# Kernel tuning notes

Measured on AMD Instinct MI355X. Metric: run time of the kernel, lower is better.

## Reference

```python
import jax, jax.numpy as jnp
import numpy as np

B, H, S, D = 2, 12, 2048, 64


def setup_inputs() -> dict:
    key = jax.random.key(0)
    kq, kk, kv = jax.random.split(key, 3)
    q = jax.random.normal(kq, (B, H, S, D), dtype=jnp.float32)
    k = jax.random.normal(kk, (B, H, S, D), dtype=jnp.float32)
    v = jax.random.normal(kv, (B, H, S, D), dtype=jnp.float32)
    # causal mask: True = attend (keep), lower triangle
    mask = jnp.tril(jnp.ones((S, S), dtype=bool))
    return {"q": q, "k": k, "v": v, "mask": mask}


def reference(q, k, v, mask):
    dim = q.shape[-1]
    # [B,H,S,S] scores
    scores = jnp.einsum("bhqd,bhkd->bhqk", q, k) / jnp.sqrt(jnp.asarray(dim, q.dtype))
    # dynamic mask-direction logic from the original module:
    # if the mask is denser in the strict upper triangle, True means "mask out";
    # otherwise True means "keep".
    sq = mask.shape[-1]
    sample = mask.reshape(-1, sq, sq)[0]
    upper = jnp.triu(jnp.ones_like(sample, dtype=bool), k=1)
    flip = jnp.sum(sample & upper) > jnp.sum(sample & ~upper)
    keep = jnp.where(flip, ~mask, mask)  # True = keep
    neg_inf = jnp.asarray(-jnp.inf, scores.dtype)
    scores = jnp.where(keep, scores, neg_inf)
    weights = jax.nn.softmax(scores, axis=-1)
    # dropout with p_drop=0.0 is the identity
    return jnp.einsum("bhqk,bhkd->bhqd", weights, v)
```

## Files before the change

kernel.cpp:

```cpp
#include <hip/hip_runtime.h>
#include <hip/hip_bf16.h>


#define SEQ 2048
#define DH 64
#define NHEADS 24
#define BN 64
#define LDK 72
#define ELEMS_PER_TENSOR (NHEADS * SEQ * DH)
#define NSLOT5 (NHEADS * 16 * 4)
#define WS_BF16  ((size_t)3 * ELEMS_PER_TENSOR * 2)
#define WS_FA5   (WS_BF16 + (size_t)NSLOT5 * 8192 * 4 + (size_t)NSLOT5 * 128 * 4)

typedef float f32x4 __attribute__((ext_vector_type(4)));
typedef __bf16 bf16x8 __attribute__((ext_vector_type(8)));
typedef __bf16 bf16x4 __attribute__((ext_vector_type(4)));

#if __has_builtin(__builtin_amdgcn_exp2f)
#define EXP2F(x) __builtin_amdgcn_exp2f(x)
#else
#define EXP2F(x) exp2f(x)
#endif

#define QSCALE 0.1803368801111204f

__global__ __launch_bounds__(256)
void prep_kernel(const float* __restrict__ q, const float* __restrict__ k,
                 const float* __restrict__ v,
                 __bf16* __restrict__ qs, __bf16* __restrict__ ks,
                 __bf16* __restrict__ vt)
{
    __shared__ __bf16 T[64][LDK];
    const int bx = blockIdx.x;
    const int tid = threadIdx.x;
    if (bx < 3072) {
        const int t = bx * 256 + tid;
        const int half = ELEMS_PER_TENSOR / 8;
        const bool is_q = t < half;
        const int idx = (is_q ? t : t - half) * 8;
        const float* src = is_q ? q : k;
        const float sc = is_q ? QSCALE : 1.0f;
        f32x4 a = *(const f32x4*)(src + idx);
        f32x4 b = *(const f32x4*)(src + idx + 4);
        bf16x8 o;
        #pragma unroll
        for (int j = 0; j < 4; ++j) { o[j] = (__bf16)(a[j] * sc); o[4 + j] = (__bf16)(b[j] * sc); }
        *(bf16x8*)((is_q ? qs : ks) + idx) = o;
    } else {
        const int b2 = bx - 3072;
        const int bh = b2 >> 5;
        const int s0 = (b2 & 31) * 64;
        const int r = tid >> 2, c0 = (tid & 3) * 16;
        const float* vp = v + (size_t)bh * SEQ * DH + (size_t)(s0 + r) * DH + c0;
        __bf16 tmp[16];
        #pragma unroll
        for (int jj = 0; jj < 16; ++jj) tmp[jj] = (__bf16)vp[jj];
        *(bf16x8*)&T[r][c0]     = *(bf16x8*)&tmp[0];
        *(bf16x8*)&T[r][c0 + 8] = *(bf16x8*)&tmp[8];
        __syncthreads();
        const int d = tid >> 2, j0 = (tid & 3) * 16;
        __bf16 o[16];
        #pragma unroll
        for (int jj = 0; jj < 16; ++jj) o[jj] = T[j0 + jj][d];
        __bf16* op = vt + (size_t)bh * DH * SEQ + (size_t)d * SEQ + s0 + j0;
        *(bf16x8*)op       = *(bf16x8*)&o[0];
        *(bf16x8*)(op + 8) = *(bf16x8*)&o[8];
    }
}

__global__ __launch_bounds__(256, 4)
void fa5_kernel(const __bf16* __restrict__ qs, const __bf16* __restrict__ ks,
                const __bf16* __restrict__ vt,
                float* __restrict__ opart, float* __restrict__ lpart)
{
    const int bx = blockIdx.x;
    const int bh = bx / 40;
    const int rem = 39 - (bx % 40);
    int mt2, st;
    if      (rem >= 36) { mt2 = 15; st = 36; }
    else if (rem >= 32) { mt2 = 14; st = 32; }
    else if (rem >= 28) { mt2 = 13; st = 28; }
    else if (rem >= 24) { mt2 = 12; st = 24; }
    else if (rem >= 21) { mt2 = 11; st = 21; }
    else if (rem >= 18) { mt2 = 10; st = 18; }
    else if (rem >= 15) { mt2 = 9;  st = 15; }
    else if (rem >= 12) { mt2 = 8;  st = 12; }
    else if (rem >= 10) { mt2 = 7;  st = 10; }
    else if (rem >= 8)  { mt2 = 6;  st = 8; }
    else if (rem >= 6)  { mt2 = 5;  st = 6; }
    else if (rem >= 4)  { mt2 = 4;  st = 4; }
    else                { mt2 = rem; st = rem; }
    const int chunk = rem - st;
    const int jt0 = chunk * 8;
    const int jt_end = min(jt0 + 8, 2 * mt2 + 2);
    const int q0 = mt2 * 128;

    const int tid = threadIdx.x;
    const int w = tid >> 6, lane = tid & 63;
    const int g = lane >> 4, li = lane & 15;

    __shared__ __bf16 Ks[64 * 64];
    __shared__ __bf16 Vs[64 * 64];
    __shared__ __bf16 Ps[4 * 32 * 64];

    const __bf16* qh = qs + (size_t)bh * SEQ * DH;
    const __bf16* kh = ks + (size_t)bh * SEQ * DH;
    const __bf16* vh = vt + (size_t)bh * DH * SEQ;

    bf16x8 qf[2][2];
    #pragma unroll
    for (int a = 0; a < 2; ++a) {
        const __bf16* qp = qh + (size_t)(q0 + w * 32 + a * 16 + li) * DH + g * 8;
        qf[a][0] = *(const bf16x8*)qp;
        qf[a][1] = *(const bf16x8*)(qp + 32);
    }

    bf16x8 ones;
    #pragma unroll
    for (int j = 0; j < 8; ++j) ones[j] = (__bf16)1.0f;

    f32x4 acc[2][4] = {};
    f32x4 accl[2] = {};

    const int srow0 = tid >> 3;
    const int sg    = tid & 7;

    bf16x8 kr[2], vr[2];
    #pragma unroll
    for (int s = 0; s < 2; ++s) {
        const int row = s * 32 + srow0;
        const int lg = sg ^ (row & 7);
        kr[s] = *(const bf16x8*)(kh + (size_t)(jt0 * BN + row) * DH + lg * 8);
        vr[s] = *(const bf16x8*)(vh + (size_t)row * SEQ + jt0 * BN + lg * 8);
    }
    #pragma unroll
    for (int s = 0; s < 2; ++s) {
        *(bf16x8*)((char*)Ks + s * 4096 + tid * 16) = kr[s];
        *(bf16x8*)((char*)Vs + s * 4096 + tid * 16) = vr[s];
    }
    __syncthreads();

    for (int jt = jt0; jt < jt_end; ++jt) {
        if (jt + 1 < jt_end) {
            const int kv1 = (jt + 1) * BN;
            #pragma unroll
            for (int s = 0; s < 2; ++s) {
                const int row = s * 32 + srow0;
                const int lg = sg ^ (row & 7);
                kr[s] = *(const bf16x8*)(kh + (size_t)(kv1 + row) * DH + lg * 8);
                vr[s] = *(const bf16x8*)(vh + (size_t)row * SEQ + kv1 + lg * 8);
            }
        }

        float s4[2][4][4];
        #pragma unroll
        for (int t = 0; t < 4; ++t) {
            f32x4 sa0 = {}, sa1 = {};
            #pragma unroll
            for (int c = 0; c < 2; ++c) {
                bf16x8 kf = *(const bf16x8*)((const char*)Ks +
                    (t * 16 + li) * 128 + (((c * 4 + g) ^ (li & 7)) << 4));
                sa0 = __builtin_amdgcn_mfma_f32_16x16x32_bf16(kf, qf[0][c], sa0, 0, 0, 0);
                sa1 = __builtin_amdgcn_mfma_f32_16x16x32_bf16(kf, qf[1][c], sa1, 0, 0, 0);
            }
            #pragma unroll
            for (int r = 0; r < 4; ++r) { s4[0][t][r] = sa0[r]; s4[1][t][r] = sa1[r]; }
        }

        if (jt >= 2 * mt2) {
            #pragma unroll
            for (int a = 0; a < 2; ++a) {
                const int qr = q0 + w * 32 + a * 16 + li;
                #pragma unroll
                for (int t = 0; t < 4; ++t) {
                    #pragma unroll
                    for (int r = 0; r < 4; ++r)
                        if (jt * 64 + t * 16 + g * 4 + r > qr) s4[a][t][r] = -1e30f;
                }
            }
        }

        #pragma unroll
        for (int a = 0; a < 2; ++a) {
            const int row = a * 16 + li;
            #pragma unroll
            for (int t = 0; t < 4; ++t) {
                bf16x4 p4;
                #pragma unroll
                for (int r = 0; r < 4; ++r) p4[r] = (__bf16)EXP2F(s4[a][t][r]);
                const int pg = (t * 2 + (g >> 1)) ^ (li & 7);
                *(bf16x4*)((char*)Ps + w * 4096 + row * 128 + (pg << 4) + ((g & 1) << 3)) = p4;
            }
        }

        #pragma unroll
        for (int c = 0; c < 2; ++c) {
            const int pgp = ((c * 4 + g) ^ (li & 7)) << 4;
            bf16x8 pf0 = *(const bf16x8*)((const char*)Ps + w * 4096 + li * 128 + pgp);
            bf16x8 pf1 = *(const bf16x8*)((const char*)Ps + w * 4096 + (16 + li) * 128 + pgp);
            accl[0] = __builtin_amdgcn_mfma_f32_16x16x32_bf16(pf0, ones, accl[0], 0, 0, 0);
            accl[1] = __builtin_amdgcn_mfma_f32_16x16x32_bf16(pf1, ones, accl[1], 0, 0, 0);
            #pragma unroll
            for (int t = 0; t < 4; ++t) {
                bf16x8 vf = *(const bf16x8*)((const char*)Vs +
                    (t * 16 + li) * 128 + pgp);
                acc[0][t] = __builtin_amdgcn_mfma_f32_16x16x32_bf16(pf0, vf, acc[0][t], 0, 0, 0);
                acc[1][t] = __builtin_amdgcn_mfma_f32_16x16x32_bf16(pf1, vf, acc[1][t], 0, 0, 0);
            }
        }

        if (jt + 1 < jt_end) {
            __syncthreads();
            #pragma unroll
            for (int s = 0; s < 2; ++s) {
                *(bf16x8*)((char*)Ks + s * 4096 + tid * 16) = kr[s];
                *(bf16x8*)((char*)Vs + s * 4096 + tid * 16) = vr[s];
            }
            __syncthreads();
        }
    }

    const int slot = (bh * 16 + mt2) * 4 + chunk;
    float* po = opart + (size_t)slot * 8192;
    #pragma unroll
    for (int a = 0; a < 2; ++a) {
        #pragma unroll
        for (int r = 0; r < 4; ++r) {
            const int row = w * 32 + a * 16 + g * 4 + r;
            float* op = po + row * 64 + li;
            #pragma unroll
            for (int t = 0; t < 4; ++t) op[t * 16] = acc[a][t][r];
            if (li == 0) lpart[(size_t)slot * 128 + row] = accl[a][r];
        }
    }
}

__global__ __launch_bounds__(256)
void fa_reduce(const float* __restrict__ opart, const float* __restrict__ lpart,
               float* __restrict__ out)
{
    const int bx = blockIdx.x;
    const int bh = bx >> 4, mt2 = bx & 15;
    const int nc = (mt2 >> 2) + 1;
    const int base = (bh * 16 + mt2) * 4;
    const int tid = threadIdx.x;
    #pragma unroll
    for (int rnd = 0; rnd < 8; ++rnd) {
        const int flat = rnd * 1024 + tid * 4;
        const int row = flat >> 6;
        f32x4 o = {};
        float l = 0.0f;
        for (int c = 0; c < nc; ++c) {
            o += *(const f32x4*)(opart + (size_t)(base + c) * 8192 + flat);
            l += lpart[(size_t)(base + c) * 128 + row];
        }
        const float inv = 1.0f / l;
        f32x4 res = { o[0] * inv, o[1] * inv, o[2] * inv, o[3] * inv };
        *(f32x4*)(out + (size_t)bh * SEQ * DH + (size_t)mt2 * 8192 + flat) = res;
    }
}

__global__ __launch_bounds__(256, 2)
void fa_causal_kernel(const float* __restrict__ q, const float* __restrict__ k,
                      const float* __restrict__ v, float* __restrict__ out)
{
    const int mt = 31 - (blockIdx.x & 31);
    const int bh = blockIdx.x >> 5;
    const int tid = threadIdx.x;
    const int w = tid >> 6, lane = tid & 63;
    const int g = lane >> 4, li = lane & 15;
    const int m0 = mt * 64;
    __shared__ __bf16 KsF[BN][LDK];
    __shared__ __bf16 VsF[DH][LDK];
    __shared__ __bf16 PsF[4][16][LDK];
    const size_t head_off = (size_t)bh * SEQ * DH;
    const float* qh = q + head_off;
    const float* kh = k + head_off;
    const float* vh = v + head_off;
    float* oh = out + head_off;
    const int qrow = m0 + w * 16 + li;
    bf16x8 qf[2];
    {
        const float* qp = qh + (size_t)qrow * DH + g * 8;
        #pragma unroll
        for (int c = 0; c < 2; ++c) {
            const float* p = qp + c * 32;
            #pragma unroll
            for (int jj = 0; jj < 8; ++jj) qf[c][jj] = (__bf16)p[jj];
        }
    }
    f32x4 acc[4] = {};
    float mrow[4], lrow[4];
    #pragma unroll
    for (int r = 0; r < 4; ++r) { mrow[r] = -1e30f; lrow[r] = 0.0f; }
    const float scale = 0.125f;
    const int srow = tid >> 2, scol = (tid & 3) * 16;
    for (int jt = 0; jt <= mt; ++jt) {
        const int kv0 = jt * BN;
        __syncthreads();
        {
            const float* kp = kh + (size_t)(kv0 + srow) * DH + scol;
            __bf16 tmp[16];
            #pragma unroll
            for (int jj = 0; jj < 16; ++jj) tmp[jj] = (__bf16)kp[jj];
            *(bf16x8*)&KsF[srow][scol]     = *(bf16x8*)&tmp[0];
            *(bf16x8*)&KsF[srow][scol + 8] = *(bf16x8*)&tmp[8];
            const float* vp = vh + (size_t)(kv0 + srow) * DH + scol;
            #pragma unroll
            for (int jj = 0; jj < 16; ++jj) VsF[scol + jj][srow] = (__bf16)vp[jj];
        }
        __syncthreads();
        float s4[4][4];
        #pragma unroll
        for (int t = 0; t < 4; ++t) {
            f32x4 sa = {};
            #pragma unroll
            for (int c = 0; c < 2; ++c) {
                bf16x8 kfr = *(const bf16x8*)&KsF[t * 16 + li][c * 32 + g * 8];
                sa = __builtin_amdgcn_mfma_f32_16x16x32_bf16(qf[c], kfr, sa, 0, 0, 0);
            }
            #pragma unroll
            for (int r = 0; r < 4; ++r) s4[t][r] = sa[r] * scale;
        }
        if (jt == mt) {
            #pragma unroll
            for (int t = 0; t < 4; ++t) {
                const int col = kv0 + t * 16 + li;
                #pragma unroll
                for (int r = 0; r < 4; ++r)
                    if (col > m0 + w * 16 + g * 4 + r) s4[t][r] = -1e30f;
            }
        }
        #pragma unroll
        for (int r = 0; r < 4; ++r) {
            float mx = fmaxf(fmaxf(s4[0][r], s4[1][r]), fmaxf(s4[2][r], s4[3][r]));
            #pragma unroll
            for (int off = 1; off < 16; off <<= 1)
                mx = fmaxf(mx, __shfl_xor(mx, off, 64));
            const float mnew = fmaxf(mrow[r], mx);
            const float alpha = __expf(mrow[r] - mnew);
            mrow[r] = mnew;
            float ps = 0.0f;
            #pragma unroll
            for (int t = 0; t < 4; ++t) {
                const float p = __expf(s4[t][r] - mnew);
                s4[t][r] = p;
                ps += p;
            }
            #pragma unroll
            for (int off = 1; off < 16; off <<= 1)
                ps += __shfl_xor(ps, off, 64);
            lrow[r] = lrow[r] * alpha + ps;
            #pragma unroll
            for (int t = 0; t < 4; ++t) acc[t][r] *= alpha;
        }
        #pragma unroll
        for (int t = 0; t < 4; ++t)
            #pragma unroll
            for (int r = 0; r < 4; ++r)
                PsF[w][g * 4 + r][t * 16 + li] = (__bf16)s4[t][r];
        __syncthreads();
        #pragma unroll
        for (int c = 0; c < 2; ++c) {
            bf16x8 pf = *(const bf16x8*)&PsF[w][li][c * 32 + g * 8];
            #pragma unroll
            for (int t = 0; t < 4; ++t) {
                bf16x8 vfr = *(const bf16x8*)&VsF[t * 16 + li][c * 32 + g * 8];
                acc[t] = __builtin_amdgcn_mfma_f32_16x16x32_bf16(pf, vfr, acc[t], 0, 0, 0);
            }
        }
    }
    #pragma unroll
    for (int r = 0; r < 4; ++r) {
        const int row = m0 + w * 16 + g * 4 + r;
        const float inv = 1.0f / lrow[r];
        float* op = oh + (size_t)row * DH + li;
        #pragma unroll
        for (int t = 0; t < 4; ++t) op[t * 16] = acc[t][r] * inv;
    }
}

extern "C" void kernel_launch(void* const* d_in, const int* in_sizes, int n_in,
                              void* d_out, int out_size, void* d_ws, size_t ws_size,
                              hipStream_t stream) {
    (void)in_sizes; (void)n_in; (void)out_size;
    const float* q = (const float*)d_in[0];
    const float* k = (const float*)d_in[1];
    const float* v = (const float*)d_in[2];
    float* out = (float*)d_out;

    if (ws_size >= WS_FA5) {
        __bf16* qs = (__bf16*)d_ws;
        __bf16* ks = qs + ELEMS_PER_TENSOR;
        __bf16* vt = ks + ELEMS_PER_TENSOR;
        float* opart = (float*)((char*)d_ws + WS_BF16);
        float* lpart = opart + (size_t)NSLOT5 * 8192;
        prep_kernel<<<dim3(3072 + 768), dim3(256), 0, stream>>>(q, k, v, qs, ks, vt);
        fa5_kernel<<<dim3(NHEADS * 40), dim3(256), 0, stream>>>(qs, ks, vt, opart, lpart);
        fa_reduce<<<dim3(NHEADS * 16), dim3(256), 0, stream>>>(opart, lpart, out);
    } else {
        fa_causal_kernel<<<dim3(NHEADS * 32), dim3(256), 0, stream>>>(q, k, v, out);
    }
}
```

Before: 149.5 us.

## Double-buffer K/V tiles, store partial outputs in bf16, remap blocks per XCD

Turns the single-buffered K/V shared-memory tiles into double buffers with a two-tile-ahead register prefetch. This removes one of the two barriers per key tile and lets global loads overlap compute. The partial outputs written by the split kernel and read by the reduce kernel are now bf16 instead of fp32, halving that traffic at some cost in accumulation precision. It also remaps the block index so that all blocks of a head land on the same XCD for L2 locality, and lowers the occupancy hint from 4 to 3 blocks per CU because of the larger LDS footprint.

```diff
diff --git a/kernel.cpp b/kernel.cpp
--- a/kernel.cpp
+++ b/kernel.cpp
@@ -10,7 +10,7 @@
 #define ELEMS_PER_TENSOR (NHEADS * SEQ * DH)
 #define NSLOT5 (NHEADS * 16 * 4)
 #define WS_BF16  ((size_t)3 * ELEMS_PER_TENSOR * 2)
-#define WS_FA5   (WS_BF16 + (size_t)NSLOT5 * 8192 * 4 + (size_t)NSLOT5 * 128 * 4)
+#define WS_FA7   (WS_BF16 + (size_t)NSLOT5 * 8192 * 2 + (size_t)NSLOT5 * 128 * 4)
 
 typedef float f32x4 __attribute__((ext_vector_type(4)));
 typedef __bf16 bf16x8 __attribute__((ext_vector_type(8)));
@@ -68,14 +68,16 @@
     }
 }
 
-__global__ __launch_bounds__(256, 4)
-void fa5_kernel(const __bf16* __restrict__ qs, const __bf16* __restrict__ ks,
+__global__ __launch_bounds__(256, 3)
+void fa7_kernel(const __bf16* __restrict__ qs, const __bf16* __restrict__ ks,
                 const __bf16* __restrict__ vt,
-                float* __restrict__ opart, float* __restrict__ lpart)
+                __bf16* __restrict__ opart, float* __restrict__ lpart)
 {
     const int bx = blockIdx.x;
-    const int bh = bx / 40;
-    const int rem = 39 - (bx % 40);
+    const int xcd = bx & 7;
+    const int sub = bx >> 3;
+    const int bh = (sub / 40) * 8 + xcd;
+    const int rem = 39 - (sub % 40);
     int mt2, st;
     if      (rem >= 36) { mt2 = 15; st = 36; }
     else if (rem >= 32) { mt2 = 14; st = 32; }
@@ -99,8 +101,8 @@
     const int w = tid >> 6, lane = tid & 63;
     const int g = lane >> 4, li = lane & 15;
 
-    __shared__ __bf16 Ks[64 * 64];
-    __shared__ __bf16 Vs[64 * 64];
+    __shared__ __bf16 Ks[2][64 * 64];
+    __shared__ __bf16 Vs[2][64 * 64];
     __shared__ __bf16 Ps[4 * 32 * 64];
 
     const __bf16* qh = qs + (size_t)bh * SEQ * DH;
@@ -135,30 +137,50 @@
     }
     #pragma unroll
     for (int s = 0; s < 2; ++s) {
-        *(bf16x8*)((char*)Ks + s * 4096 + tid * 16) = kr[s];
-        *(bf16x8*)((char*)Vs + s * 4096 + tid * 16) = vr[s];
+        *(bf16x8*)((char*)Ks[0] + s * 4096 + tid * 16) = kr[s];
+        *(bf16x8*)((char*)Vs[0] + s * 4096 + tid * 16) = vr[s];
+    }
+    if (jt0 + 1 < jt_end) {
+        const int kv1 = (jt0 + 1) * BN;
+        #pragma unroll
+        for (int s = 0; s < 2; ++s) {
+            const int row = s * 32 + srow0;
+            const int lg = sg ^ (row & 7);
+            kr[s] = *(const bf16x8*)(kh + (size_t)(kv1 + row) * DH + lg * 8);
+            vr[s] = *(const bf16x8*)(vh + (size_t)row * SEQ + kv1 + lg * 8);
+        }
     }
     __syncthreads();
 
+    int buf = 0;
     for (int jt = jt0; jt < jt_end; ++jt) {
         if (jt + 1 < jt_end) {
-            const int kv1 = (jt + 1) * BN;
+            #pragma unroll
+            for (int s = 0; s < 2; ++s) {
+                *(bf16x8*)((char*)Ks[buf ^ 1] + s * 4096 + tid * 16) = kr[s];
+                *(bf16x8*)((char*)Vs[buf ^ 1] + s * 4096 + tid * 16) = vr[s];
+            }
+        }
+        if (jt + 2 < jt_end) {
+            const int kv2 = (jt + 2) * BN;
             #pragma unroll
             for (int s = 0; s < 2; ++s) {
                 const int row = s * 32 + srow0;
                 const int lg = sg ^ (row & 7);
-                kr[s] = *(const bf16x8*)(kh + (size_t)(kv1 + row) * DH + lg * 8);
-                vr[s] = *(const bf16x8*)(vh + (size_t)row * SEQ + kv1 + lg * 8);
-            }
-        }
-
+                kr[s] = *(const bf16x8*)(kh + (size_t)(kv2 + row) * DH + lg * 8);
+                vr[s] = *(const bf16x8*)(vh + (size_t)row * SEQ + kv2 + lg * 8);
+            }
+        }
+
+        const char* Kb = (const char*)Ks[buf];
+        const char* Vb = (const char*)Vs[buf];
         float s4[2][4][4];
         #pragma unroll
         for (int t = 0; t < 4; ++t) {
             f32x4 sa0 = {}, sa1 = {};
             #pragma unroll
             for (int c = 0; c < 2; ++c) {
-                bf16x8 kf = *(const bf16x8*)((const char*)Ks +
+                bf16x8 kf = *(const bf16x8*)(Kb +
                     (t * 16 + li) * 128 + (((c * 4 + g) ^ (li & 7)) << 4));
                 sa0 = __builtin_amdgcn_mfma_f32_16x16x32_bf16(kf, qf[0][c], sa0, 0, 0, 0);
                 sa1 = __builtin_amdgcn_mfma_f32_16x16x32_bf16(kf, qf[1][c], sa1, 0, 0, 0);
@@ -202,41 +224,33 @@
             accl[1] = __builtin_amdgcn_mfma_f32_16x16x32_bf16(pf1, ones, accl[1], 0, 0, 0);
             #pragma unroll
             for (int t = 0; t < 4; ++t) {
-                bf16x8 vf = *(const bf16x8*)((const char*)Vs +
-                    (t * 16 + li) * 128 + pgp);
+                bf16x8 vf = *(const bf16x8*)(Vb + (t * 16 + li) * 128 + pgp);
                 acc[0][t] = __builtin_amdgcn_mfma_f32_16x16x32_bf16(pf0, vf, acc[0][t], 0, 0, 0);
                 acc[1][t] = __builtin_amdgcn_mfma_f32_16x16x32_bf16(pf1, vf, acc[1][t], 0, 0, 0);
             }
         }
 
-        if (jt + 1 < jt_end) {
-            __syncthreads();
-            #pragma unroll
-            for (int s = 0; s < 2; ++s) {
-                *(bf16x8*)((char*)Ks + s * 4096 + tid * 16) = kr[s];
-                *(bf16x8*)((char*)Vs + s * 4096 + tid * 16) = vr[s];
-            }
-            __syncthreads();
-        }
+        if (jt + 1 < jt_end) __syncthreads();
+        buf ^= 1;
     }
 
     const int slot = (bh * 16 + mt2) * 4 + chunk;
-    float* po = opart + (size_t)slot * 8192;
+    __bf16* po = opart + (size_t)slot * 8192;
     #pragma unroll
     for (int a = 0; a < 2; ++a) {
         #pragma unroll
         for (int r = 0; r < 4; ++r) {
             const int row = w * 32 + a * 16 + g * 4 + r;
-            float* op = po + row * 64 + li;
-            #pragma unroll
-            for (int t = 0; t < 4; ++t) op[t * 16] = acc[a][t][r];
+            __bf16* op = po + row * 64 + li;
+            #pragma unroll
+            for (int t = 0; t < 4; ++t) op[t * 16] = (__bf16)acc[a][t][r];
             if (li == 0) lpart[(size_t)slot * 128 + row] = accl[a][r];
         }
     }
 }
 
 __global__ __launch_bounds__(256)
-void fa_reduce(const float* __restrict__ opart, const float* __restrict__ lpart,
+void fa_reduce(const __bf16* __restrict__ opart, const float* __restrict__ lpart,
                float* __restrict__ out)
 {
     const int bx = blockIdx.x;
@@ -248,14 +262,14 @@
     for (int rnd = 0; rnd < 8; ++rnd) {
         const int flat = rnd * 1024 + tid * 4;
         const int row = flat >> 6;
-        f32x4 o = {};
-        float l = 0.0f;
+        float o0 = 0, o1 = 0, o2 = 0, o3 = 0, l = 0;
         for (int c = 0; c < nc; ++c) {
-            o += *(const f32x4*)(opart + (size_t)(base + c) * 8192 + flat);
+            bf16x4 ov = *(const bf16x4*)(opart + (size_t)(base + c) * 8192 + flat);
+            o0 += (float)ov[0]; o1 += (float)ov[1]; o2 += (float)ov[2]; o3 += (float)ov[3];
             l += lpart[(size_t)(base + c) * 128 + row];
         }
         const float inv = 1.0f / l;
-        f32x4 res = { o[0] * inv, o[1] * inv, o[2] * inv, o[3] * inv };
+        f32x4 res = { o0 * inv, o1 * inv, o2 * inv, o3 * inv };
         *(f32x4*)(out + (size_t)bh * SEQ * DH + (size_t)mt2 * 8192 + flat) = res;
     }
 }
@@ -389,14 +403,14 @@
     const float* v = (const float*)d_in[2];
     float* out = (float*)d_out;
 
-    if (ws_size >= WS_FA5) {
+    if (ws_size >= WS_FA7) {
         __bf16* qs = (__bf16*)d_ws;
         __bf16* ks = qs + ELEMS_PER_TENSOR;
         __bf16* vt = ks + ELEMS_PER_TENSOR;
-        float* opart = (float*)((char*)d_ws + WS_BF16);
-        float* lpart = opart + (size_t)NSLOT5 * 8192;
+        __bf16* opart = (__bf16*)((char*)d_ws + WS_BF16);
+        float* lpart = (float*)((char*)d_ws + WS_BF16 + (size_t)NSLOT5 * 8192 * 2);
         prep_kernel<<<dim3(3072 + 768), dim3(256), 0, stream>>>(q, k, v, qs, ks, vt);
-        fa5_kernel<<<dim3(NHEADS * 40), dim3(256), 0, stream>>>(qs, ks, vt, opart, lpart);
+        fa7_kernel<<<dim3(NHEADS * 40), dim3(256), 0, stream>>>(qs, ks, vt, opart, lpart);
         fa_reduce<<<dim3(NHEADS * 16), dim3(256), 0, stream>>>(opart, lpart, out);
     } else {
         fa_causal_kernel<<<dim3(NHEADS * 32), dim3(256), 0, stream>>>(q, k, v, out);
```

Result: faster. 133.5 us (-10.7%).
